# Performance work log

Measured on AMD Instinct MI355X. Metric: run time of the kernel, lower is better.

The kernel has to match this reference:

```python
import jax, jax.numpy as jnp
import numpy as np

D_MODEL = 512
NUM_HEADS = 8
DEPTH = D_MODEL // NUM_HEADS
B, S = 8, 1024


def setup_inputs() -> dict:
    key = jax.random.key(0)
    ks = jax.random.split(key, 14)
    scale = 1.0 / np.sqrt(D_MODEL)
    inp = {
        "q_in": jax.random.normal(ks[0], (B, S, D_MODEL), jnp.float32),
        "k_in": jax.random.normal(ks[1], (B, S, D_MODEL), jnp.float32),
        "v_in": jax.random.normal(ks[2], (B, S, D_MODEL), jnp.float32),
        # padding mask: 1 = masked-out position
        "mask": jax.random.randint(ks[3], (B, 1, 1, S), 0, 2).astype(jnp.float32),
        "additional_weights": jax.random.uniform(ks[4], (B, S, S), jnp.float32),
        "wq": jax.random.normal(ks[5], (D_MODEL, D_MODEL), jnp.float32) * scale,
        "bq": jnp.zeros((D_MODEL,), jnp.float32),
        "wk": jax.random.normal(ks[6], (D_MODEL, D_MODEL), jnp.float32) * scale,
        "bk": jnp.zeros((D_MODEL,), jnp.float32),
        "wv": jax.random.normal(ks[7], (D_MODEL, D_MODEL), jnp.float32) * scale,
        "bv": jnp.zeros((D_MODEL,), jnp.float32),
        "wo": jax.random.normal(ks[8], (D_MODEL, D_MODEL), jnp.float32) * scale,
        "bo": jnp.zeros((D_MODEL,), jnp.float32),
    }
    return inp


def _split_heads(x):
    # [B, S, d_model] -> [B, H, S, depth]
    b, s, _ = x.shape
    return x.reshape(b, s, NUM_HEADS, DEPTH).transpose(0, 2, 1, 3)


def reference(q_in, k_in, v_in, mask, additional_weights,
              wq, bq, wk, bk, wv, bv, wo, bo):
    q = _split_heads(q_in @ wq + bq)  # [B,H,S,D]
    k = _split_heads(k_in @ wk + bk)
    v = _split_heads(v_in @ wv + bv)

    scores = jnp.einsum("bhqd,bhkd->bhqk", q, k) / jnp.sqrt(
        jnp.asarray(DEPTH, q.dtype))
    scores = scores + mask * -1e9
    attn = jax.nn.softmax(scores, axis=-1)
    # post-softmax multiplicative weights, broadcast over heads
    attn = attn * additional_weights[:, None, :, :]
    x = jnp.einsum("bhqk,bhkd->bhqd", attn, v)
    x = x.transpose(0, 2, 1, 3).reshape(q_in.shape[0], -1, D_MODEL)
    out = x @ wo + bo
    return out, attn
```

## Files before the change

### kernel.cpp

```cpp
#include <hip/hip_runtime.h>
#include <stdint.h>

typedef unsigned short u16;
typedef short bf16x8 __attribute__((ext_vector_type(8)));
typedef float f32x4 __attribute__((ext_vector_type(4)));
typedef u16 u16x8 __attribute__((ext_vector_type(8)));
typedef u16 u16x4 __attribute__((ext_vector_type(4)));

#define NHEADS 8
#define SEQ 1024
#define DM 512
#define DEPTH 64
#define BATCH 8
#define PSTRIDE 1032

__device__ __forceinline__ u16 f2bf(float f) {
    union { float f; unsigned u; } v; v.f = f;
    unsigned r = v.u + 0x7FFF + ((v.u >> 16) & 1);
    return (u16)(r >> 16);
}

__global__ void __launch_bounds__(256) transpose512(
    const float* __restrict__ w0, const float* __restrict__ w1,
    const float* __restrict__ w2, const float* __restrict__ w3,
    u16* __restrict__ wt)
{
    __shared__ float tile[32][33];
    const float* w = (blockIdx.z == 0) ? w0 : (blockIdx.z == 1) ? w1
                   : (blockIdx.z == 2) ? w2 : w3;
    u16* o = wt + (size_t)blockIdx.z * (DM * DM);
    int rb = blockIdx.y * 32, cb = blockIdx.x * 32;
    int tx = threadIdx.x, ty = threadIdx.y;
    #pragma unroll
    for (int k = 0; k < 32; k += 8)
        tile[ty + k][tx] = w[(size_t)(rb + ty + k) * DM + cb + tx];
    __syncthreads();
    #pragma unroll
    for (int k = 0; k < 32; k += 8)
        o[(size_t)(cb + ty + k) * DM + rb + tx] = f2bf(tile[tx][ty + k]);
}

__global__ void __launch_bounds__(256) conv_bf16(
    const float* __restrict__ q, const float* __restrict__ k,
    const float* __restrict__ v,
    u16* __restrict__ oq, u16* __restrict__ ok, u16* __restrict__ ov)
{
    const float* src = (blockIdx.z == 0) ? q : (blockIdx.z == 1) ? k : v;
    u16* dst = (blockIdx.z == 0) ? oq : (blockIdx.z == 1) ? ok : ov;
    size_t i = ((size_t)blockIdx.x * 256 + threadIdx.x) * 8;
    f32x4 a = *(const f32x4*)(src + i);
    f32x4 b = *(const f32x4*)(src + i + 4);
    u16x8 o;
    #pragma unroll
    for (int j = 0; j < 4; j++) { o[j] = f2bf(a[j]); o[j + 4] = f2bf(b[j]); }
    *(u16x8*)(dst + i) = o;
}

template <int LAYOUT>
__device__ __forceinline__ void gemm_tile(
    const u16* __restrict__ A, const u16* __restrict__ wt,
    const float* __restrict__ bias, void* __restrict__ out_)
{
    const int tid = threadIdx.x;
    const int wid = tid >> 6, lane = tid & 63;
    const int wm = wid >> 1, wn = wid & 1;
    const int mb = blockIdx.y * 128 + wm * 64;
    const int nb = blockIdx.x * 128 + wn * 64;
    const int lr = lane & 15, g = lane >> 4, lk = g * 8;

    f32x4 acc[4][4];
    #pragma unroll
    for (int i = 0; i < 4; i++)
        #pragma unroll
        for (int j = 0; j < 4; j++) acc[i][j] = (f32x4)0.f;

    for (int ks = 0; ks < DM; ks += 32) {
        bf16x8 a[4], bf[4];
        #pragma unroll
        for (int mt = 0; mt < 4; mt++)
            a[mt] = *(const bf16x8*)(A + (size_t)(mb + mt * 16 + lr) * DM + ks + lk);
        #pragma unroll
        for (int nt = 0; nt < 4; nt++)
            bf[nt] = *(const bf16x8*)(wt + (size_t)(nb + nt * 16 + lr) * DM + ks + lk);
        #pragma unroll
        for (int mt = 0; mt < 4; mt++)
            #pragma unroll
            for (int nt = 0; nt < 4; nt++) {
                if (LAYOUT == 1)
                    acc[mt][nt] = __builtin_amdgcn_mfma_f32_16x16x32_bf16(
                        bf[nt], a[mt], acc[mt][nt], 0, 0, 0);
                else
                    acc[mt][nt] = __builtin_amdgcn_mfma_f32_16x16x32_bf16(
                        a[mt], bf[nt], acc[mt][nt], 0, 0, 0);
            }
    }

    #pragma unroll
    for (int mt = 0; mt < 4; mt++) {
        #pragma unroll
        for (int nt = 0; nt < 4; nt++) {
            #pragma unroll
            for (int r = 0; r < 4; r++) {
                if (LAYOUT == 1) {
                    int m = mb + mt * 16 + lr;
                    int n = nb + nt * 16 + 4 * g + r;
                    float val = acc[mt][nt][r] + bias[n];
                    int b_ = m >> 10, s = m & 1023, h = n >> 6, d = n & 63;
                    ((u16*)out_)[((size_t)((b_ * NHEADS + h) << 6) + d) * SEQ + s] = f2bf(val);
                } else {
                    int n = nb + nt * 16 + lr;
                    int m = mb + mt * 16 + 4 * g + r;
                    float val = acc[mt][nt][r] + bias[n];
                    if (LAYOUT == 2) {
                        ((float*)out_)[(size_t)m * DM + n] = val;
                    } else {
                        int b_ = m >> 10, s = m & 1023, h = n >> 6, d = n & 63;
                        ((u16*)out_)[(((size_t)(b_ * NHEADS + h) * SEQ + s) << 6) + d] = f2bf(val);
                    }
                }
            }
        }
    }
}

__global__ void __launch_bounds__(256) qkv_proj(
    const u16* __restrict__ qbf, const u16* __restrict__ kbf,
    const u16* __restrict__ vbf, const u16* __restrict__ wt_base,
    const float* __restrict__ bq, const float* __restrict__ bk,
    const float* __restrict__ bv,
    u16* __restrict__ Qb, u16* __restrict__ Kb, u16* __restrict__ VTb)
{
    int z = blockIdx.z;
    if (z == 0)      gemm_tile<0>(qbf, wt_base,               bq, Qb);
    else if (z == 1) gemm_tile<0>(kbf, wt_base + DM * DM,     bk, Kb);
    else             gemm_tile<1>(vbf, wt_base + 2 * DM * DM, bv, VTb);
}

__global__ void __launch_bounds__(256) out_proj(
    const u16* __restrict__ X, const u16* __restrict__ wto,
    const float* __restrict__ bo, float* __restrict__ out)
{
    gemm_tile<2>(X, wto, bo, out);
}

__global__ void __launch_bounds__(256) attn_kernel(
    const u16* __restrict__ Q, const u16* __restrict__ K,
    const u16* __restrict__ VT, const float* __restrict__ mask,
    const float* __restrict__ addw, float* __restrict__ attn_out,
    u16* __restrict__ X)
{
    __shared__ u16 Pl[16 * PSTRIDE];
    __shared__ float redm[4][16];
    __shared__ float reds[4][16];

    const int id = blockIdx.x;
    const int c = id & 7, t = id >> 3;
    const int h = t & 7;
    const int p = ((t >> 3) << 3) | c;
    const int qt = p & 63, b = p >> 6;

    const int tid = threadIdx.x, wid = tid >> 6, lane = tid & 63;
    const int lr = lane & 15, g = lane >> 4, lk = g * 8;
    const size_t head = (size_t)(b * NHEADS + h) * (SEQ * DEPTH);
    const u16* Qh = Q + head + (size_t)qt * 16 * DEPTH;
    const u16* Kh = K + head;
    const u16* Vh = VT + head;
    const int wbase = wid << 8;

    bf16x8 qf0 = *(const bf16x8*)(Qh + lr * DEPTH + lk);
    bf16x8 qf1 = *(const bf16x8*)(Qh + lr * DEPTH + 32 + lk);
    f32x4 acc[16];
    #pragma unroll
    for (int nt = 0; nt < 16; nt++) acc[nt] = (f32x4)0.f;
    #pragma unroll
    for (int nt = 0; nt < 16; nt++) {
        const u16* kp = Kh + (size_t)(wbase + (nt << 4) + lr) * DEPTH + lk;
        bf16x8 k0 = *(const bf16x8*)kp;
        bf16x8 k1 = *(const bf16x8*)(kp + 32);
        acc[nt] = __builtin_amdgcn_mfma_f32_16x16x32_bf16(k0, qf0, acc[nt], 0, 0, 0);
        acc[nt] = __builtin_amdgcn_mfma_f32_16x16x32_bf16(k1, qf1, acc[nt], 0, 0, 0);
    }

    const float* mrow = mask + ((size_t)b << 10);
    float mx = -3.0e38f;
    #pragma unroll
    for (int nt = 0; nt < 16; nt++) {
        f32x4 mr = *(const f32x4*)(mrow + wbase + (nt << 4) + 4 * g);
        #pragma unroll
        for (int r = 0; r < 4; r++) {
            acc[nt][r] = acc[nt][r] * 0.125f + mr[r] * -1e9f;
            mx = fmaxf(mx, acc[nt][r]);
        }
    }
    mx = fmaxf(mx, __shfl_xor(mx, 16, 64));
    mx = fmaxf(mx, __shfl_xor(mx, 32, 64));
    if (lane < 16) redm[wid][lr] = mx;
    __syncthreads();
    float gm = fmaxf(fmaxf(redm[0][lr], redm[1][lr]),
                     fmaxf(redm[2][lr], redm[3][lr]));

    float sm = 0.f;
    #pragma unroll
    for (int nt = 0; nt < 16; nt++)
        #pragma unroll
        for (int r = 0; r < 4; r++) {
            float pv = __expf(acc[nt][r] - gm);
            acc[nt][r] = pv;
            sm += pv;
        }
    sm += __shfl_xor(sm, 16, 64);
    sm += __shfl_xor(sm, 32, 64);
    if (lane < 16) reds[wid][lr] = sm;
    __syncthreads();
    float iv = 1.0f / (reds[0][lr] + reds[1][lr] + reds[2][lr] + reds[3][lr]);

    const int qglob = (qt << 4) + lr;
    const size_t awbase = ((size_t)((b << 10) + qglob)) << 10;
    const size_t aobase = ((size_t)(((b * NHEADS + h) << 10) + qglob)) << 10;
    #pragma unroll
    for (int nt = 0; nt < 16; nt++) {
        int k0 = wbase + (nt << 4) + 4 * g;
        f32x4 aw = *(const f32x4*)(addw + awbase + k0);
        f32x4 o;
        u16x4 pb;
        #pragma unroll
        for (int r = 0; r < 4; r++) {
            float v = acc[nt][r] * iv * aw[r];
            o[r] = v;
            pb[r] = f2bf(v);
        }
        *(f32x4*)(attn_out + aobase + k0) = o;
        *(u16x4*)(Pl + lr * PSTRIDE + k0) = pb;
    }
    __syncthreads();

    f32x4 x = (f32x4)0.f;
    const u16* vrow = Vh + (size_t)((wid << 4) + lr) * SEQ;
    for (int ks = 0; ks < SEQ; ks += 32) {
        bf16x8 a = *(const bf16x8*)(Pl + lr * PSTRIDE + ks + lk);
        bf16x8 bv = *(const bf16x8*)(vrow + ks + lk);
        x = __builtin_amdgcn_mfma_f32_16x16x32_bf16(a, bv, x, 0, 0, 0);
    }
    int d = (h << 6) + (wid << 4) + lr;
    #pragma unroll
    for (int r = 0; r < 4; r++)
        X[((size_t)((b << 10) + (qt << 4) + 4 * g + r)) * DM + d] = f2bf(x[r]);
}

extern "C" void kernel_launch(void* const* d_in, const int* in_sizes, int n_in,
                              void* d_out, int out_size, void* d_ws, size_t ws_size,
                              hipStream_t stream)
{
    const float* q_in = (const float*)d_in[0];
    const float* k_in = (const float*)d_in[1];
    const float* v_in = (const float*)d_in[2];
    const float* mask = (const float*)d_in[3];
    const float* addw = (const float*)d_in[4];
    const float* wq = (const float*)d_in[5];
    const float* bq = (const float*)d_in[6];
    const float* wk = (const float*)d_in[7];
    const float* bk = (const float*)d_in[8];
    const float* wv = (const float*)d_in[9];
    const float* bv = (const float*)d_in[10];
    const float* wo = (const float*)d_in[11];
    const float* bo = (const float*)d_in[12];

    const size_t ACT = (size_t)BATCH * SEQ * DM;

    u16* ws = (u16*)d_ws;
    u16* wt  = ws;
    u16* Qb  = wt + 4 * DM * DM;
    u16* Kb  = Qb + ACT;
    u16* VTb = Kb + ACT;
    u16* Xb  = VTb + ACT;

    float* out0 = (float*)d_out;
    float* attn_out = out0 + ACT;

    u16* qbf = (u16*)attn_out;
    u16* kbf = qbf + ACT;
    u16* vbf = kbf + ACT;

    transpose512<<<dim3(16, 16, 4), dim3(32, 8), 0, stream>>>(wq, wk, wv, wo, wt);
    conv_bf16<<<dim3(2048, 1, 3), 256, 0, stream>>>(q_in, k_in, v_in, qbf, kbf, vbf);
    qkv_proj<<<dim3(4, 64, 3), 256, 0, stream>>>(qbf, kbf, vbf, wt, bq, bk, bv,
                                                 Qb, Kb, VTb);
    attn_kernel<<<dim3(4096), 256, 0, stream>>>(Qb, Kb, VTb, mask, addw,
                                                attn_out, Xb);
    out_proj<<<dim3(4, 64, 1), 256, 0, stream>>>(Xb, wt + 3 * DM * DM, bo, out0);
}
```

Before: 582.6 us.

## Compute PV directly from score registers, dropping shared P buffer

The attention kernel now interleaves the key assignment across waves so that each wave's softmax-output accumulator layout matches the A-operand layout of a 16x16x16 bf16 MFMA. P·V is computed straight from registers instead of staging the full 16x1024 P tile in shared memory. Each wave covers all 64 depth columns over its own key subset, and the four partial results are reduced through a small shared buffer. This frees about 33KB of LDS per block (launch bounds now request 5 blocks per SM) and removes one barrier-separated phase. In exchange it uses a narrower MFMA, issues more scattered 8-byte V loads, and adds a cross-wave reduction.

```diff
diff --git a/kernel.cpp b/kernel.cpp
--- a/kernel.cpp
+++ b/kernel.cpp
@@ -3,6 +3,7 @@
 
 typedef unsigned short u16;
 typedef short bf16x8 __attribute__((ext_vector_type(8)));
+typedef short bf16x4 __attribute__((ext_vector_type(4)));
 typedef float f32x4 __attribute__((ext_vector_type(4)));
 typedef u16 u16x8 __attribute__((ext_vector_type(8)));
 typedef u16 u16x4 __attribute__((ext_vector_type(4)));
@@ -12,12 +13,20 @@
 #define DM 512
 #define DEPTH 64
 #define BATCH 8
-#define PSTRIDE 1032
 
 __device__ __forceinline__ u16 f2bf(float f) {
     union { float f; unsigned u; } v; v.f = f;
     unsigned r = v.u + 0x7FFF + ((v.u >> 16) & 1);
     return (u16)(r >> 16);
+}
+
+__device__ __forceinline__ f32x4 mfma_16x16x16_bf16(bf16x4 a, bf16x4 b, f32x4 c) {
+#if __has_builtin(__builtin_amdgcn_mfma_f32_16x16x16bf16_1k)
+    return __builtin_amdgcn_mfma_f32_16x16x16bf16_1k(a, b, c, 0, 0, 0);
+#else
+    asm("v_mfma_f32_16x16x16_bf16 %0, %1, %2, %0" : "+v"(c) : "v"(a), "v"(b));
+    return c;
+#endif
 }
 
 __global__ void __launch_bounds__(256) transpose512(
@@ -143,13 +152,13 @@
     gemm_tile<2>(X, wto, bo, out);
 }
 
-__global__ void __launch_bounds__(256) attn_kernel(
+__global__ void __launch_bounds__(256, 5) attn_kernel(
     const u16* __restrict__ Q, const u16* __restrict__ K,
     const u16* __restrict__ VT, const float* __restrict__ mask,
     const float* __restrict__ addw, float* __restrict__ attn_out,
     u16* __restrict__ X)
 {
-    __shared__ u16 Pl[16 * PSTRIDE];
+    __shared__ float Xr[4][16][64];
     __shared__ float redm[4][16];
     __shared__ float reds[4][16];
 
@@ -165,7 +174,7 @@
     const u16* Qh = Q + head + (size_t)qt * 16 * DEPTH;
     const u16* Kh = K + head;
     const u16* Vh = VT + head;
-    const int wbase = wid << 8;
+    const int kst = (wid << 4) + (g << 2);
 
     bf16x8 qf0 = *(const bf16x8*)(Qh + lr * DEPTH + lk);
     bf16x8 qf1 = *(const bf16x8*)(Qh + lr * DEPTH + 32 + lk);
@@ -174,7 +183,7 @@
     for (int nt = 0; nt < 16; nt++) acc[nt] = (f32x4)0.f;
     #pragma unroll
     for (int nt = 0; nt < 16; nt++) {
-        const u16* kp = Kh + (size_t)(wbase + (nt << 4) + lr) * DEPTH + lk;
+        const u16* kp = Kh + (size_t)(nt * 64 + (wid << 4) + lr) * DEPTH + lk;
         bf16x8 k0 = *(const bf16x8*)kp;
         bf16x8 k1 = *(const bf16x8*)(kp + 32);
         acc[nt] = __builtin_amdgcn_mfma_f32_16x16x32_bf16(k0, qf0, acc[nt], 0, 0, 0);
@@ -185,7 +194,7 @@
     float mx = -3.0e38f;
     #pragma unroll
     for (int nt = 0; nt < 16; nt++) {
-        f32x4 mr = *(const f32x4*)(mrow + wbase + (nt << 4) + 4 * g);
+        f32x4 mr = *(const f32x4*)(mrow + nt * 64 + kst);
         #pragma unroll
         for (int r = 0; r < 4; r++) {
             acc[nt][r] = acc[nt][r] * 0.125f + mr[r] * -1e9f;
@@ -217,34 +226,45 @@
     const int qglob = (qt << 4) + lr;
     const size_t awbase = ((size_t)((b << 10) + qglob)) << 10;
     const size_t aobase = ((size_t)(((b * NHEADS + h) << 10) + qglob)) << 10;
+    const u16* vb_base = Vh + (size_t)lr * SEQ;
+
+    f32x4 x[4];
+    #pragma unroll
+    for (int dt = 0; dt < 4; dt++) x[dt] = (f32x4)0.f;
+
     #pragma unroll
     for (int nt = 0; nt < 16; nt++) {
-        int k0 = wbase + (nt << 4) + 4 * g;
+        const int k0 = nt * 64 + kst;
         f32x4 aw = *(const f32x4*)(addw + awbase + k0);
         f32x4 o;
-        u16x4 pb;
+        bf16x4 pa;
         #pragma unroll
         for (int r = 0; r < 4; r++) {
             float v = acc[nt][r] * iv * aw[r];
             o[r] = v;
-            pb[r] = f2bf(v);
+            pa[r] = (short)f2bf(v);
         }
         *(f32x4*)(attn_out + aobase + k0) = o;
-        *(u16x4*)(Pl + lr * PSTRIDE + k0) = pb;
-    }
+        #pragma unroll
+        for (int dt = 0; dt < 4; dt++) {
+            bf16x4 vb = *(const bf16x4*)(vb_base + (size_t)(dt << 4) * SEQ + k0);
+            x[dt] = mfma_16x16x16_bf16(pa, vb, x[dt]);
+        }
+    }
+
+    #pragma unroll
+    for (int dt = 0; dt < 4; dt++)
+        #pragma unroll
+        for (int r = 0; r < 4; r++)
+            Xr[wid][4 * g + r][(dt << 4) + lr] = x[dt][r];
     __syncthreads();
 
-    f32x4 x = (f32x4)0.f;
-    const u16* vrow = Vh + (size_t)((wid << 4) + lr) * SEQ;
-    for (int ks = 0; ks < SEQ; ks += 32) {
-        bf16x8 a = *(const bf16x8*)(Pl + lr * PSTRIDE + ks + lk);
-        bf16x8 bv = *(const bf16x8*)(vrow + ks + lk);
-        x = __builtin_amdgcn_mfma_f32_16x16x32_bf16(a, bv, x, 0, 0, 0);
-    }
-    int d = (h << 6) + (wid << 4) + lr;
-    #pragma unroll
-    for (int r = 0; r < 4; r++)
-        X[((size_t)((b << 10) + (qt << 4) + 4 * g + r)) * DM + d] = f2bf(x[r]);
+    #pragma unroll
+    for (int r = 0; r < 4; r++) {
+        int q = 4 * g + r, d = (wid << 4) + lr;
+        float s = Xr[0][q][d] + Xr[1][q][d] + Xr[2][q][d] + Xr[3][q][d];
+        X[((size_t)((b << 10) + (qt << 4) + q)) * DM + (h << 6) + d] = f2bf(s);
+    }
 }
 
 extern "C" void kernel_launch(void* const* d_in, const int* in_sizes, int n_in,
```

New measurement: 659.3 us. +13.2%, slower.
